# Kernel tuning notes

Measured on AMD Instinct MI355X. Metric: run time of the kernel, lower is better.

## Reference

```python
import jax, jax.numpy as jnp
import numpy as np

LN_EPS = 1e-5

def _layernorm(x, g, b):
    mu = x.mean(-1, keepdims=True)
    var = ((x - mu) ** 2).mean(-1, keepdims=True)
    return (x - mu) * jax.lax.rsqrt(var + LN_EPS) * g + b

def setup_inputs() -> dict:
    key = jax.random.key(0)
    ks = jax.random.split(key, 5)
    B, S, H, V = 1, 1024, 768, 50257
    return {
        "hidden_states": jax.random.normal(ks[0], (B, S, H), jnp.float32),
        "attention_mask": jnp.ones((B, S), jnp.int32),
        "alpha": jnp.float32(0.1),
        "ln_gamma": jnp.ones((H,), jnp.float32),
        "ln_beta": jnp.zeros((H,), jnp.float32),
        "W1": jax.random.normal(ks[1], (H, H), jnp.float32) * 0.02,
        "b1": jnp.zeros((H,), jnp.float32),
        "W2": jax.random.normal(ks[2], (H, H), jnp.float32) * 0.02,
        "b2": jnp.zeros((H,), jnp.float32),
        "lm_head_w": jax.random.normal(ks[3], (V, H), jnp.float32) * 0.02,
        "n_processors": 4,
        "k_steps": 4,
    }

def reference(hidden_states, attention_mask, alpha, ln_gamma, ln_beta,
              W1, b1, W2, b2, lm_head_w, n_processors, k_steps):
    P = int(n_processors)
    K = int(k_steps)
    mask = attention_mask.astype(hidden_states.dtype)[..., None]        # [B,S,1]
    # processor_states: [P,B,S,H] (all initialized to the same hidden state)
    states = jnp.broadcast_to(hidden_states[None], (P,) + hidden_states.shape)
    for _ in range(K):
        # eval mode: dropout=identity, no noise -> mutate == mask multiply
        mut = states * mask                                             # [P,B,S,H]
        if P > 1:
            # mean of other processors = (sum_all - self)/(P-1)
            observe = (mut.sum(0, keepdims=True) - mut) / (P - 1)
        else:
            observe = jnp.zeros_like(mut)
        merged = mut + alpha * observe
        normed = _layernorm(merged, ln_gamma, ln_beta)
        h = jax.nn.gelu(jnp.einsum('pbsh,ih->pbsi', normed, W1) + b1,
                        approximate=False)
        delta = jnp.einsum('pbsi,hi->pbsh', h, W2) + b2
        states = (mut + delta) * mask
    consensus = states.mean(0)                                          # [B,S,H]
    logits = jnp.einsum('bsh,vh->bsv', consensus, lm_head_w)            # [B,S,V]
    processor_logits = jnp.einsum('pbsh,vh->pbsv', states, lm_head_w)   # [P,B,S,V]
    return logits, processor_logits, states
```

## Files before the change

kernel.cpp:

```cpp
#include <hip/hip_runtime.h>
#include <hip/hip_bf16.h>
#include <math.h>

#define S_LEN 1024
#define HDIM  768
#define NPROC 4
#define VOCAB 50257
#define KSTEPS 4

typedef __attribute__((ext_vector_type(4))) float f32x4;
typedef __attribute__((ext_vector_type(8))) short bf16x8;
typedef __attribute__((ext_vector_type(4))) short short4v;

static __device__ __forceinline__ ushort f2bf(float f) {
  union { __hip_bfloat16 b; ushort u; } cv;
  cv.b = __float2bfloat16(f);
  return cv.u;
}

#define GLOAD16(gp, lp) __builtin_amdgcn_global_load_lds( \
    (const __attribute__((address_space(1))) unsigned int*)(gp), \
    (__attribute__((address_space(3))) unsigned int*)(lp), 16, 0, 0)

__global__ void cvt_bf16(const float* __restrict__ in, ushort* __restrict__ out, int n4) {
  const int i = blockIdx.x * 256 + threadIdx.x;
  if (i >= n4) return;
  f32x4 v = ((const f32x4*)in)[i];
  short4v o;
#pragma unroll
  for (int j = 0; j < 4; j++) o[j] = (short)f2bf(v[j]);
  ((short4v*)out)[i] = o;
}

__global__ void copy_f32(const float* __restrict__ in, float* __restrict__ out) {
  const int i = blockIdx.x * 256 + threadIdx.x;
  ((f32x4*)out)[i] = ((const f32x4*)in)[i];
}

__global__ void expand_states(const float* __restrict__ st1, float* __restrict__ out) {
  const int i = blockIdx.x * 256 + threadIdx.x;
  f32x4 v = ((const f32x4*)st1)[i];
#pragma unroll
  for (int p = 0; p < NPROC; p++) ((f32x4*)out)[(size_t)p * (S_LEN * HDIM / 4) + i] = v;
}

__global__ __launch_bounds__(256) void bcast_logits(
    const float* __restrict__ src, float* __restrict__ dst) {
  const size_t n4 = (size_t)S_LEN * VOCAB / 4;
  for (size_t i = (size_t)blockIdx.x * 256 + threadIdx.x; i < n4;
       i += (size_t)gridDim.x * 256) {
    f32x4 v = ((const f32x4*)src)[i];
#pragma unroll
    for (int p = 0; p < NPROC; p++)
      ((f32x4*)dst)[(size_t)p * n4 + i] = v;
  }
}

__global__ __launch_bounds__(256) void merge_ln_p1(
    const float* __restrict__ st1, const int* __restrict__ mask,
    const float* __restrict__ alphap, const float* __restrict__ gamma,
    const float* __restrict__ beta, ushort* __restrict__ normed) {
  const int s = blockIdx.x;
  const int tid = threadIdx.x;
  const float mk = (float)mask[s];
  const float a1 = 1.0f + alphap[0];
  float merged[3];
  float lsum = 0.f, lsq = 0.f;
#pragma unroll
  for (int e = 0; e < 3; e++) {
    const int h = tid + e * 256;
    float mg = st1[(size_t)s * HDIM + h] * mk * a1;
    merged[e] = mg;
    lsum += mg;
    lsq += mg * mg;
  }
#pragma unroll
  for (int off = 32; off > 0; off >>= 1) {
    lsum += __shfl_down(lsum, off, 64);
    lsq  += __shfl_down(lsq, off, 64);
  }
  __shared__ float rs_[4], rq_[4];
  const int wv = tid >> 6, ln = tid & 63;
  if (ln == 0) { rs_[wv] = lsum; rq_[wv] = lsq; }
  __syncthreads();
  const float ts = rs_[0] + rs_[1] + rs_[2] + rs_[3];
  const float tq = rq_[0] + rq_[1] + rq_[2] + rq_[3];
  const float mu = ts * (1.f / HDIM);
  const float var = tq * (1.f / HDIM) - mu * mu;
  const float rstd = rsqrtf(var + 1e-5f);
#pragma unroll
  for (int e = 0; e < 3; e++) {
    const int h = tid + e * 256;
    float nv = (merged[e] - mu) * rstd * gamma[h] + beta[h];
    normed[(size_t)s * HDIM + h] = f2bf(nv);
  }
}

template <int MODE>
__global__ __launch_bounds__(256, 4) void gemm_mlp(
    const ushort* __restrict__ A, const ushort* __restrict__ B,
    const float* __restrict__ bias, ushort* __restrict__ out_bf,
    float* __restrict__ states, const int* __restrict__ mask) {
  __shared__ __align__(16) ushort lsA[2][4096];
  __shared__ __align__(16) ushort lsB[2][2048];
  const int tid = threadIdx.x;
  const int bx = blockIdx.x;
  const int mt = bx & 7;
  const int nt = bx >> 3;
  const int wv = tid >> 6, lane = tid & 63;
  const int wm = wv >> 1, wn = wv & 1;
  const int g = lane >> 4, lr = lane & 15;

  f32x4 acc[4][2];
#pragma unroll
  for (int i = 0; i < 4; i++)
#pragma unroll
    for (int j = 0; j < 2; j++) acc[i][j] = (f32x4){0.f, 0.f, 0.f, 0.f};

  const int koff = (tid & 3) * 8;
  const int arow0 = mt * 128 + (tid >> 2);
  const ushort* gA0 = A + (size_t)arow0 * HDIM + koff;
  const ushort* gA1 = gA0 + (size_t)64 * HDIM;
  const ushort* gB0 = B + (size_t)(nt * 64 + (tid >> 2)) * HDIM + koff;
  const int dst = (tid >> 2) * 32 + (tid & 3) * 8;

#define STAGE(kt, buf) do {                      \
    const int o_ = (kt) * 32;                    \
    GLOAD16(gA0 + o_, &lsA[buf][dst]);           \
    GLOAD16(gA1 + o_, &lsA[buf][2048 + dst]);    \
    GLOAD16(gB0 + o_, &lsB[buf][dst]);           \
  } while (0)

  constexpr int NT = HDIM / 32;
  STAGE(0, 0);
  STAGE(1, 1);
  int cur = 0;
  for (int kt = 0; kt < NT; ++kt) {
    if (kt < NT - 1) asm volatile("s_waitcnt vmcnt(3)" ::: "memory");
    else             asm volatile("s_waitcnt vmcnt(0)" ::: "memory");
    __builtin_amdgcn_s_barrier();
    __builtin_amdgcn_sched_barrier(0);
    bf16x8 af[4], bfr[2];
#pragma unroll
    for (int mi = 0; mi < 4; mi++)
      af[mi] = *(const bf16x8*)(&lsA[cur][(wm * 64 + mi * 16 + lr) * 32 + g * 8]);
#pragma unroll
    for (int ni = 0; ni < 2; ni++)
      bfr[ni] = *(const bf16x8*)(&lsB[cur][(wn * 32 + ni * 16 + lr) * 32 + g * 8]);
    asm volatile("s_waitcnt lgkmcnt(0)" ::: "memory");
    __builtin_amdgcn_sched_barrier(0);
    __builtin_amdgcn_s_setprio(1);
#pragma unroll
    for (int mi = 0; mi < 4; mi++)
#pragma unroll
      for (int ni = 0; ni < 2; ni++)
        acc[mi][ni] = __builtin_amdgcn_mfma_f32_16x16x32_bf16(af[mi], bfr[ni], acc[mi][ni], 0, 0, 0);
    __builtin_amdgcn_s_setprio(0);
    __builtin_amdgcn_s_barrier();
    __builtin_amdgcn_sched_barrier(0);
    if (kt + 2 < NT) STAGE(kt + 2, cur);
    cur ^= 1;
  }
#undef STAGE

#pragma unroll
  for (int mi = 0; mi < 4; mi++) {
    const int mrow = mt * 128 + wm * 64 + mi * 16 + g * 4;
#pragma unroll
    for (int ni = 0; ni < 2; ni++) {
      const int ncol = nt * 64 + wn * 32 + ni * 16 + lr;
      const float bv = bias[ncol];
      if (MODE == 0) {
#pragma unroll
        for (int j = 0; j < 4; j++) {
          float x = acc[mi][ni][j] + bv;
          float ge = 0.5f * x * (1.f + erff(x * 0.70710678118654752f));
          out_bf[(size_t)(mrow + j) * HDIM + ncol] = f2bf(ge);
        }
      } else {
#pragma unroll
        for (int j = 0; j < 4; j++) {
          const int m = mrow + j;
          const float mk = (float)mask[m];
          const size_t idx = (size_t)m * HDIM + ncol;
          const float mut = states[idx] * mk;
          const float ns = (mut + acc[mi][ni][j] + bv) * mk;
          states[idx] = ns;
          if (out_bf) out_bf[idx] = f2bf(ns);
        }
      }
    }
  }
}

__global__ __launch_bounds__(512, 2) void gemm_lm(
    const ushort* __restrict__ A, const ushort* __restrict__ B,
    float* __restrict__ logits, int nrowsB) {
  __shared__ __align__(16) ushort lds[2][4][8192];
  ushort* ldsb = &lds[0][0][0];
  const int tid = threadIdx.x;
  const int bx = blockIdx.x;
  const int mt = bx & 3;
  const int nt = bx >> 2;
  const int wv = tid >> 6, lane = tid & 63;
  const int wm = wv >> 2, wn = wv & 3;
  const int g = lane >> 4, lr = lane & 15;

  f32x4 acc[8][4];
#pragma unroll
  for (int i = 0; i < 8; i++)
#pragma unroll
    for (int j = 0; j < 4; j++) acc[i][j] = (f32x4){0.f, 0.f, 0.f, 0.f};

  const ushort* gsrc[4][2];
#pragma unroll
  for (int j = 0; j < 2; j++) {
    const int c = j * 512 + wv * 64 + lane;
    const int qa = c >> 9, ra = (c >> 3) & 63, oa = (c & 7) ^ (ra & 7);
    gsrc[0][j] = A + (size_t)(mt * 256 + qa * 128 + ra) * HDIM + oa * 8;
    gsrc[1][j] = A + (size_t)(mt * 256 + qa * 128 + 64 + ra) * HDIM + oa * 8;
    const int qb = c >> 8, rb = (c >> 3) & 31, ob = (c & 7) ^ (rb & 7);
    int r2 = nt * 256 + qb * 64 + rb;      if (r2 >= nrowsB) r2 = nrowsB - 1;
    int r3 = nt * 256 + qb * 64 + 32 + rb; if (r3 >= nrowsB) r3 = nrowsB - 1;
    gsrc[2][j] = B + (size_t)r2 * HDIM + ob * 8;
    gsrc[3][j] = B + (size_t)r3 * HDIM + ob * 8;
  }
  const int a_lane = wm * 4096 + lr * 64;
  const int b_lane = wn * 2048 + lr * 64;
  int slot8[2];
  slot8[0] = ((0 + g) ^ (lr & 7)) * 8;
  slot8[1] = ((4 + g) ^ (lr & 7)) * 8;

#define STG(R_, tt_) do {                                                     \
    ushort* dst_ = ldsb + (size_t)((((tt_) & 1) * 4 + (R_)) * 8192 + wv * 512); \
    GLOAD16(gsrc[R_][0] + (size_t)(tt_) * 64, dst_);                          \
    GLOAD16(gsrc[R_][1] + (size_t)(tt_) * 64, dst_ + 4096);                   \
  } while (0)

#define MFMA_Q(MB, NB, AV, BV) do {                                           \
    __builtin_amdgcn_s_setprio(1);                                           \
    _Pragma("unroll")                                                        \
    for (int mi = 0; mi < 4; mi++)                                           \
      _Pragma("unroll")                                                      \
      for (int ni = 0; ni < 2; ni++)                                         \
        _Pragma("unroll")                                                    \
        for (int ks = 0; ks < 2; ks++)                                       \
          acc[(MB) + mi][(NB) + ni] = __builtin_amdgcn_mfma_f32_16x16x32_bf16( \
              AV[mi][ks], BV[ni][ks], acc[(MB) + mi][(NB) + ni], 0, 0, 0);   \
    __builtin_amdgcn_s_setprio(0);                                           \
  } while (0)

  constexpr int NT = HDIM / 64;
  STG(0, 0); STG(2, 0); STG(3, 0); STG(1, 0);
  asm volatile("s_waitcnt vmcnt(4)" ::: "memory");
  __builtin_amdgcn_sched_barrier(0);
  __builtin_amdgcn_s_barrier();

  bf16x8 af[4][2], blo[2][2], bhi[2][2];
  for (int t = 0; t < NT - 1; ++t) {
    const ushort* cp = ldsb + (size_t)(t & 1) * 32768;
#pragma unroll
    for (int mi = 0; mi < 4; mi++)
#pragma unroll
      for (int ks = 0; ks < 2; ks++)
        af[mi][ks] = *(const bf16x8*)(cp + a_lane + mi * 1024 + slot8[ks]);
#pragma unroll
    for (int ni = 0; ni < 2; ni++)
#pragma unroll
      for (int ks = 0; ks < 2; ks++)
        blo[ni][ks] = *(const bf16x8*)(cp + 16384 + b_lane + ni * 1024 + slot8[ks]);
    STG(0, t + 1);
    __builtin_amdgcn_s_barrier();
    asm volatile("s_waitcnt lgkmcnt(0)" ::: "memory");
    __builtin_amdgcn_sched_barrier(0);
    MFMA_Q(0, 0, af, blo);
    asm volatile("s_waitcnt vmcnt(4)" ::: "memory");
    __builtin_amdgcn_sched_barrier(0);
    __builtin_amdgcn_s_barrier();
#pragma unroll
    for (int ni = 0; ni < 2; ni++)
#pragma unroll
      for (int ks = 0; ks < 2; ks++)
        bhi[ni][ks] = *(const bf16x8*)(cp + 24576 + b_lane + ni * 1024 + slot8[ks]);
    STG(2, t + 1);
    __builtin_amdgcn_s_barrier();
    asm volatile("s_waitcnt lgkmcnt(0)" ::: "memory");
    __builtin_amdgcn_sched_barrier(0);
    MFMA_Q(0, 2, af, bhi);
    asm volatile("s_waitcnt vmcnt(4)" ::: "memory");
    __builtin_amdgcn_sched_barrier(0);
    __builtin_amdgcn_s_barrier();
#pragma unroll
    for (int mi = 0; mi < 4; mi++)
#pragma unroll
      for (int ks = 0; ks < 2; ks++)
        af[mi][ks] = *(const bf16x8*)(cp + 8192 + a_lane + mi * 1024 + slot8[ks]);
    STG(3, t + 1);
    __builtin_amdgcn_s_barrier();
    asm volatile("s_waitcnt lgkmcnt(0)" ::: "memory");
    __builtin_amdgcn_sched_barrier(0);
    MFMA_Q(4, 2, af, bhi);
    __builtin_amdgcn_s_barrier();
    STG(1, t + 1);
    __builtin_amdgcn_s_barrier();
    MFMA_Q(4, 0, af, blo);
    asm volatile("s_waitcnt vmcnt(4)" ::: "memory");
    __builtin_amdgcn_sched_barrier(0);
    __builtin_amdgcn_s_barrier();
  }
  {
    const int t = NT - 1;
    const ushort* cp = ldsb + (size_t)(t & 1) * 32768;
#pragma unroll
    for (int mi = 0; mi < 4; mi++)
#pragma unroll
      for (int ks = 0; ks < 2; ks++)
        af[mi][ks] = *(const bf16x8*)(cp + a_lane + mi * 1024 + slot8[ks]);
#pragma unroll
    for (int ni = 0; ni < 2; ni++)
#pragma unroll
      for (int ks = 0; ks < 2; ks++)
        blo[ni][ks] = *(const bf16x8*)(cp + 16384 + b_lane + ni * 1024 + slot8[ks]);
    __builtin_amdgcn_s_barrier();
    asm volatile("s_waitcnt lgkmcnt(0)" ::: "memory");
    __builtin_amdgcn_sched_barrier(0);
    MFMA_Q(0, 0, af, blo);
    asm volatile("s_waitcnt vmcnt(2)" ::: "memory");
    __builtin_amdgcn_sched_barrier(0);
    __builtin_amdgcn_s_barrier();
#pragma unroll
    for (int ni = 0; ni < 2; ni++)
#pragma unroll
      for (int ks = 0; ks < 2; ks++)
        bhi[ni][ks] = *(const bf16x8*)(cp + 24576 + b_lane + ni * 1024 + slot8[ks]);
    __builtin_amdgcn_s_barrier();
    asm volatile("s_waitcnt lgkmcnt(0)" ::: "memory");
    __builtin_amdgcn_sched_barrier(0);
    MFMA_Q(0, 2, af, bhi);
    asm volatile("s_waitcnt vmcnt(0)" ::: "memory");
    __builtin_amdgcn_sched_barrier(0);
    __builtin_amdgcn_s_barrier();
#pragma unroll
    for (int mi = 0; mi < 4; mi++)
#pragma unroll
      for (int ks = 0; ks < 2; ks++)
        af[mi][ks] = *(const bf16x8*)(cp + 8192 + a_lane + mi * 1024 + slot8[ks]);
    asm volatile("s_waitcnt lgkmcnt(0)" ::: "memory");
    __builtin_amdgcn_sched_barrier(0);
    MFMA_Q(4, 2, af, bhi);
    MFMA_Q(4, 0, af, blo);
  }
#undef STG
#undef MFMA_Q

  float* sc = ((float*)ldsb) + wv * 1024;
  const int ncol0 = nt * 256 + wn * 64;
  const bool fast = (ncol0 + 64) <= nrowsB;
#pragma unroll
  for (int mi = 0; mi < 8; mi++) {
    __syncthreads();
#pragma unroll
    for (int ni = 0; ni < 4; ni++)
#pragma unroll
      for (int j = 0; j < 4; j++)
        sc[(g * 4 + j) * 64 + ni * 16 + lr] = acc[mi][ni][j];
    __syncthreads();
    const int srow0 = mt * 256 + wm * 128 + mi * 16;
    const int c0 = ncol0 + lr * 4;
#pragma unroll
    for (int jj = 0; jj < 4; jj++) {
      const f32x4 v = *(const f32x4*)&sc[(g * 4 + jj) * 64 + lr * 4];
      const int s = srow0 + g * 4 + jj;
      if (fast) {
        *(f32x4*)&logits[(size_t)s * VOCAB + c0] = v;
      } else {
#pragma unroll
        for (int cc = 0; cc < 4; cc++)
          if (c0 + cc < nrowsB) logits[(size_t)s * VOCAB + c0 + cc] = v[cc];
      }
    }
  }
}

extern "C" void kernel_launch(void* const* d_in, const int* in_sizes, int n_in,
                              void* d_out, int out_size, void* d_ws, size_t ws_size,
                              hipStream_t stream) {
  const float* hidden = (const float*)d_in[0];
  const int*   mask   = (const int*)d_in[1];
  const float* alphap = (const float*)d_in[2];
  const float* gamma  = (const float*)d_in[3];
  const float* beta   = (const float*)d_in[4];
  const float* W1     = (const float*)d_in[5];
  const float* b1     = (const float*)d_in[6];
  const float* W2     = (const float*)d_in[7];
  const float* b2     = (const float*)d_in[8];
  const float* lmw    = (const float*)d_in[9];

  float* logits  = (float*)d_out;
  float* plogits = logits + (size_t)S_LEN * VOCAB;
  float* states  = plogits + (size_t)NPROC * S_LEN * VOCAB;

  uint8_t* ws = (uint8_t*)d_ws;
  ushort* lm_bf  = (ushort*)ws;
  ushort* w1_bf  = (ushort*)(ws + 77194752);
  ushort* w2_bf  = (ushort*)(ws + 78374400);
  ushort* nrm_bf = (ushort*)(ws + 79554048);
  ushort* h_bf   = (ushort*)(ws + 81126912);
  ushort* a_bf   = (ushort*)(ws + 82699776);
  float*  st1    = (float*) (ws + 84272640);
  if (ws_size < 87418368) return;

  cvt_bf16<<<(VOCAB * HDIM / 4 + 255) / 256, 256, 0, stream>>>(lmw, lm_bf, VOCAB * HDIM / 4);
  cvt_bf16<<<(HDIM * HDIM / 4 + 255) / 256, 256, 0, stream>>>(W1, w1_bf, HDIM * HDIM / 4);
  cvt_bf16<<<(HDIM * HDIM / 4 + 255) / 256, 256, 0, stream>>>(W2, w2_bf, HDIM * HDIM / 4);
  copy_f32<<<S_LEN * HDIM / 4 / 256, 256, 0, stream>>>(hidden, st1);

  for (int k = 0; k < KSTEPS; k++) {
    merge_ln_p1<<<S_LEN, 256, 0, stream>>>(st1, mask, alphap, gamma, beta, nrm_bf);
    gemm_mlp<0><<<(HDIM / 64) * 8, 256, 0, stream>>>(nrm_bf, w1_bf, b1, h_bf, nullptr, nullptr);
    gemm_mlp<1><<<(HDIM / 64) * 8, 256, 0, stream>>>(
        h_bf, w2_bf, b2, (k == KSTEPS - 1) ? (ushort*)a_bf : nullptr, st1, mask);
  }
  expand_states<<<S_LEN * HDIM / 4 / 256, 256, 0, stream>>>(st1, states);
  gemm_lm<<<((VOCAB + 255) / 256) * 4, 512, 0, stream>>>(a_bf, lm_bf, logits, VOCAB);
  bcast_logits<<<2048, 256, 0, stream>>>(logits, plogits);
}
```

Before: 546.7 us.

## Fuse MLP step loop into one persistent kernel with grid barriers

Replaces the per-step merge/LayerNorm, two MLP GEMM kernels, the copy and the state-expansion kernels with one persistent kernel of 96 blocks. The phases are separated by an atomic-counter grid barrier, and the three weight-conversion launches are merged into one. The aim is to remove roughly fifteen kernel launches and their launch gaps. The cost is spin-wait barrier overhead, and the design relies on all 96 blocks being co-resident. It also reads hidden directly on the first step instead of copying it.

```diff
diff --git a/kernel.cpp b/kernel.cpp
--- a/kernel.cpp
+++ b/kernel.cpp
@@ -7,6 +7,7 @@
 #define NPROC 4
 #define VOCAB 50257
 #define KSTEPS 4
+#define LOOP_BLOCKS 96
 
 typedef __attribute__((ext_vector_type(4))) float f32x4;
 typedef __attribute__((ext_vector_type(8))) short bf16x8;
@@ -22,26 +23,24 @@
     (const __attribute__((address_space(1))) unsigned int*)(gp), \
     (__attribute__((address_space(3))) unsigned int*)(lp), 16, 0, 0)
 
-__global__ void cvt_bf16(const float* __restrict__ in, ushort* __restrict__ out, int n4) {
-  const int i = blockIdx.x * 256 + threadIdx.x;
+__global__ void prep_weights(const float* __restrict__ lmw, const float* __restrict__ W1,
+                             const float* __restrict__ W2, ushort* __restrict__ lm_bf,
+                             ushort* __restrict__ w1_bf, ushort* __restrict__ w2_bf) {
+  const int LM4 = VOCAB * HDIM / 4;
+  const int W4  = HDIM * HDIM / 4;
+  const int LMB = (LM4 + 255) / 256;
+  const int WB  = (W4 + 255) / 256;
+  const int bid = blockIdx.x;
+  const float* in; ushort* out; int n4, i;
+  if (bid < LMB)           { in = lmw; out = lm_bf; n4 = LM4; i = bid * 256 + threadIdx.x; }
+  else if (bid < LMB + WB) { in = W1;  out = w1_bf; n4 = W4;  i = (bid - LMB) * 256 + threadIdx.x; }
+  else                     { in = W2;  out = w2_bf; n4 = W4;  i = (bid - LMB - WB) * 256 + threadIdx.x; }
   if (i >= n4) return;
   f32x4 v = ((const f32x4*)in)[i];
   short4v o;
 #pragma unroll
   for (int j = 0; j < 4; j++) o[j] = (short)f2bf(v[j]);
   ((short4v*)out)[i] = o;
-}
-
-__global__ void copy_f32(const float* __restrict__ in, float* __restrict__ out) {
-  const int i = blockIdx.x * 256 + threadIdx.x;
-  ((f32x4*)out)[i] = ((const f32x4*)in)[i];
-}
-
-__global__ void expand_states(const float* __restrict__ st1, float* __restrict__ out) {
-  const int i = blockIdx.x * 256 + threadIdx.x;
-  f32x4 v = ((const f32x4*)st1)[i];
-#pragma unroll
-  for (int p = 0; p < NPROC; p++) ((f32x4*)out)[(size_t)p * (S_LEN * HDIM / 4) + i] = v;
 }
 
 __global__ __launch_bounds__(256) void bcast_logits(
@@ -56,53 +55,24 @@
   }
 }
 
-__global__ __launch_bounds__(256) void merge_ln_p1(
-    const float* __restrict__ st1, const int* __restrict__ mask,
-    const float* __restrict__ alphap, const float* __restrict__ gamma,
-    const float* __restrict__ beta, ushort* __restrict__ normed) {
-  const int s = blockIdx.x;
-  const int tid = threadIdx.x;
-  const float mk = (float)mask[s];
-  const float a1 = 1.0f + alphap[0];
-  float merged[3];
-  float lsum = 0.f, lsq = 0.f;
-#pragma unroll
-  for (int e = 0; e < 3; e++) {
-    const int h = tid + e * 256;
-    float mg = st1[(size_t)s * HDIM + h] * mk * a1;
-    merged[e] = mg;
-    lsum += mg;
-    lsq += mg * mg;
-  }
-#pragma unroll
-  for (int off = 32; off > 0; off >>= 1) {
-    lsum += __shfl_down(lsum, off, 64);
-    lsq  += __shfl_down(lsq, off, 64);
-  }
-  __shared__ float rs_[4], rq_[4];
-  const int wv = tid >> 6, ln = tid & 63;
-  if (ln == 0) { rs_[wv] = lsum; rq_[wv] = lsq; }
+static __device__ __forceinline__ void grid_barrier(int* cnt, int target) {
   __syncthreads();
-  const float ts = rs_[0] + rs_[1] + rs_[2] + rs_[3];
-  const float tq = rq_[0] + rq_[1] + rq_[2] + rq_[3];
-  const float mu = ts * (1.f / HDIM);
-  const float var = tq * (1.f / HDIM) - mu * mu;
-  const float rstd = rsqrtf(var + 1e-5f);
-#pragma unroll
-  for (int e = 0; e < 3; e++) {
-    const int h = tid + e * 256;
-    float nv = (merged[e] - mu) * rstd * gamma[h] + beta[h];
-    normed[(size_t)s * HDIM + h] = f2bf(nv);
-  }
+  if (threadIdx.x == 0) {
+    __threadfence();
+    atomicAdd(cnt, 1);
+    while (atomicAdd(cnt, 0) < target) { }
+    __threadfence();
+  }
+  __syncthreads();
 }
 
 template <int MODE>
-__global__ __launch_bounds__(256, 4) void gemm_mlp(
+static __device__ __forceinline__ void mlp_phase(
     const ushort* __restrict__ A, const ushort* __restrict__ B,
     const float* __restrict__ bias, ushort* __restrict__ out_bf,
-    float* __restrict__ states, const int* __restrict__ mask) {
-  __shared__ __align__(16) ushort lsA[2][4096];
-  __shared__ __align__(16) ushort lsB[2][2048];
+    const float* __restrict__ src, float* __restrict__ dst,
+    const int* __restrict__ mask,
+    ushort lsA[][4096], ushort lsB[][2048]) {
   const int tid = threadIdx.x;
   const int bx = blockIdx.x;
   const int mt = bx & 7;
@@ -122,13 +92,13 @@
   const ushort* gA0 = A + (size_t)arow0 * HDIM + koff;
   const ushort* gA1 = gA0 + (size_t)64 * HDIM;
   const ushort* gB0 = B + (size_t)(nt * 64 + (tid >> 2)) * HDIM + koff;
-  const int dst = (tid >> 2) * 32 + (tid & 3) * 8;
+  const int dstl = (tid >> 2) * 32 + (tid & 3) * 8;
 
 #define STAGE(kt, buf) do {                      \
     const int o_ = (kt) * 32;                    \
-    GLOAD16(gA0 + o_, &lsA[buf][dst]);           \
-    GLOAD16(gA1 + o_, &lsA[buf][2048 + dst]);    \
-    GLOAD16(gB0 + o_, &lsB[buf][dst]);           \
+    GLOAD16(gA0 + o_, &lsA[buf][dstl]);          \
+    GLOAD16(gA1 + o_, &lsA[buf][2048 + dstl]);   \
+    GLOAD16(gB0 + o_, &lsB[buf][dstl]);          \
   } while (0)
 
   constexpr int NT = HDIM / 32;
@@ -183,13 +153,77 @@
           const int m = mrow + j;
           const float mk = (float)mask[m];
           const size_t idx = (size_t)m * HDIM + ncol;
-          const float mut = states[idx] * mk;
+          const float mut = src[idx] * mk;
           const float ns = (mut + acc[mi][ni][j] + bv) * mk;
-          states[idx] = ns;
+          dst[idx] = ns;
           if (out_bf) out_bf[idx] = f2bf(ns);
         }
       }
     }
+  }
+}
+
+__global__ __launch_bounds__(256) void fused_loop(
+    const float* __restrict__ hidden, const int* __restrict__ mask,
+    const float* __restrict__ alphap, const float* __restrict__ gamma,
+    const float* __restrict__ beta,
+    const ushort* __restrict__ w1, const float* __restrict__ b1,
+    const ushort* __restrict__ w2, const float* __restrict__ b2,
+    float* __restrict__ st1, ushort* __restrict__ nrm, ushort* __restrict__ hbuf,
+    ushort* __restrict__ a_bf, float* __restrict__ states, int* __restrict__ cnt) {
+  __shared__ __align__(16) ushort lsA[2][4096];
+  __shared__ __align__(16) ushort lsB[2][2048];
+  __shared__ float rs_[4], rq_[4];
+  const int tid = threadIdx.x;
+  const float a1 = 1.0f + alphap[0];
+  int gen = 0;
+
+  for (int k = 0; k < KSTEPS; k++) {
+    const float* src = (k == 0) ? hidden : st1;
+    for (int s = blockIdx.x; s < S_LEN; s += LOOP_BLOCKS) {
+      const float mk = (float)mask[s];
+      float merged[3];
+      float lsum = 0.f, lsq = 0.f;
+#pragma unroll
+      for (int e = 0; e < 3; e++) {
+        const int h = tid + e * 256;
+        float mg = src[(size_t)s * HDIM + h] * mk * a1;
+        merged[e] = mg;
+        lsum += mg;
+        lsq += mg * mg;
+      }
+#pragma unroll
+      for (int off = 32; off > 0; off >>= 1) {
+        lsum += __shfl_down(lsum, off, 64);
+        lsq  += __shfl_down(lsq, off, 64);
+      }
+      const int wv = tid >> 6, ln = tid & 63;
+      if (ln == 0) { rs_[wv] = lsum; rq_[wv] = lsq; }
+      __syncthreads();
+      const float ts = rs_[0] + rs_[1] + rs_[2] + rs_[3];
+      const float tq = rq_[0] + rq_[1] + rq_[2] + rq_[3];
+      const float mu = ts * (1.f / HDIM);
+      const float var = tq * (1.f / HDIM) - mu * mu;
+      const float rstd = rsqrtf(var + 1e-5f);
+#pragma unroll
+      for (int e = 0; e < 3; e++) {
+        const int h = tid + e * 256;
+        float nv = (merged[e] - mu) * rstd * gamma[h] + beta[h];
+        nrm[(size_t)s * HDIM + h] = f2bf(nv);
+      }
+      __syncthreads();
+    }
+    grid_barrier(cnt, (++gen) * LOOP_BLOCKS);
+    mlp_phase<0>(nrm, w1, b1, hbuf, nullptr, nullptr, mask, lsA, lsB);
+    grid_barrier(cnt, (++gen) * LOOP_BLOCKS);
+    mlp_phase<1>(hbuf, w2, b2, (k == KSTEPS - 1) ? a_bf : nullptr, src, st1, mask, lsA, lsB);
+    grid_barrier(cnt, (++gen) * LOOP_BLOCKS);
+  }
+  for (int i = blockIdx.x * 256 + tid; i < S_LEN * HDIM / 4; i += LOOP_BLOCKS * 256) {
+    f32x4 v = ((const f32x4*)st1)[i];
+#pragma unroll
+    for (int p = 0; p < NPROC; p++)
+      ((f32x4*)states)[(size_t)p * (S_LEN * HDIM / 4) + i] = v;
   }
 }
 
@@ -408,20 +442,15 @@
   ushort* h_bf   = (ushort*)(ws + 81126912);
   ushort* a_bf   = (ushort*)(ws + 82699776);
   float*  st1    = (float*) (ws + 84272640);
-  if (ws_size < 87418368) return;
-
-  cvt_bf16<<<(VOCAB * HDIM / 4 + 255) / 256, 256, 0, stream>>>(lmw, lm_bf, VOCAB * HDIM / 4);
-  cvt_bf16<<<(HDIM * HDIM / 4 + 255) / 256, 256, 0, stream>>>(W1, w1_bf, HDIM * HDIM / 4);
-  cvt_bf16<<<(HDIM * HDIM / 4 + 255) / 256, 256, 0, stream>>>(W2, w2_bf, HDIM * HDIM / 4);
-  copy_f32<<<S_LEN * HDIM / 4 / 256, 256, 0, stream>>>(hidden, st1);
-
-  for (int k = 0; k < KSTEPS; k++) {
-    merge_ln_p1<<<S_LEN, 256, 0, stream>>>(st1, mask, alphap, gamma, beta, nrm_bf);
-    gemm_mlp<0><<<(HDIM / 64) * 8, 256, 0, stream>>>(nrm_bf, w1_bf, b1, h_bf, nullptr, nullptr);
-    gemm_mlp<1><<<(HDIM / 64) * 8, 256, 0, stream>>>(
-        h_bf, w2_bf, b2, (k == KSTEPS - 1) ? (ushort*)a_bf : nullptr, st1, mask);
-  }
-  expand_states<<<S_LEN * HDIM / 4 / 256, 256, 0, stream>>>(st1, states);
+  int*    cnt    = (int*)   (ws + 87418368);
+  if (ws_size < 87418496) return;
+
+  hipMemsetAsync(cnt, 0, 128, stream);
+  const int LMB = (VOCAB * HDIM / 4 + 255) / 256, WB = (HDIM * HDIM / 4 + 255) / 256;
+  prep_weights<<<LMB + 2 * WB, 256, 0, stream>>>(lmw, W1, W2, lm_bf, w1_bf, w2_bf);
+  fused_loop<<<LOOP_BLOCKS, 256, 0, stream>>>(
+      hidden, mask, alphap, gamma, beta, w1_bf, b1, w2_bf, b2,
+      st1, nrm_bf, h_bf, a_bf, states, cnt);
   gemm_lm<<<((VOCAB + 255) / 256) * 4, 512, 0, stream>>>(a_bf, lm_bf, logits, VOCAB);
   bcast_logits<<<2048, 256, 0, stream>>>(logits, plogits);
 }
```

Measured after the change: 664.1 us. 1.21x slower.
